# Optimization experiments

Hardware: AMD Instinct MI355X
Metric: run time of the kernel (lower is better)

## Reference

```python
import jax, jax.numpy as jnp
import numpy as np

B, A, D, H = 2048, 32, 128, 256

def setup_inputs() -> dict:
    key = jax.random.key(0)
    ks = jax.random.split(key, 12)
    s = lambda fan_in: 1.0 / np.sqrt(fan_in)
    return {
        "obs": jax.random.normal(ks[0], (B, A, D), dtype=jnp.float32),
        "act": jax.random.normal(ks[1], (B, A, 8), dtype=jnp.float32),
        "enc_W": jax.random.uniform(ks[2], (H, D), jnp.float32, -s(D), s(D)),
        "enc_b": jax.random.uniform(ks[3], (H,), jnp.float32, -s(D), s(D)),
        "fobs_W": jax.random.uniform(ks[4], (H, H), jnp.float32, -s(H), s(H)),
        "fobs_b": jax.random.uniform(ks[5], (H,), jnp.float32, -s(H), s(H)),
        "W_ih": jax.random.uniform(ks[6], (3 * H, H), jnp.float32, -s(H), s(H)),
        "b_ih": jax.random.uniform(ks[7], (3 * H,), jnp.float32, -s(H), s(H)),
        "W_hh": jax.random.uniform(ks[8], (3 * H, H), jnp.float32, -s(H), s(H)),
        "b_hh": jax.random.uniform(ks[9], (3 * H,), jnp.float32, -s(H), s(H)),
        "dec_W": jax.random.uniform(ks[10], (1, H), jnp.float32, -s(H), s(H)),
        "dec_b": jax.random.uniform(ks[11], (1,), jnp.float32, -s(H), s(H)),
    }

def _gru_cell(x, h, W_ih, b_ih, W_hh, b_hh):
    # torch.nn.GRUCell: gates stacked as [reset, update, new]
    gi = x @ W_ih.T + b_ih          # [N, 3H]
    gh = h @ W_hh.T + b_hh          # [N, 3H]
    i_r, i_z, i_n = jnp.split(gi, 3, axis=-1)
    h_r, h_z, h_n = jnp.split(gh, 3, axis=-1)
    r = jax.nn.sigmoid(i_r + h_r)
    z = jax.nn.sigmoid(i_z + h_z)
    n = jnp.tanh(i_n + r * h_n)
    return (1.0 - z) * n + z * h

def reference(obs, act, enc_W, enc_b, fobs_W, fobs_b, W_ih, b_ih, W_hh, b_hh, dec_W, dec_b):
    b, a, d = obs.shape
    x = obs.reshape(b * a, d)                         # [B*A, D]
    e = jax.nn.relu(x @ enc_W.T + enc_b)              # encoder + ReLU
    h = e @ fobs_W.T + fobs_b                         # h_out
    # k = 0: comm input is zeros
    h = _gru_cell(jnp.zeros_like(h), h, W_ih, b_ih, W_hh, b_hh)
    # k = 1: masked mean over other agents == (sum_j h_j - h_i) / n_agents
    hA = h.reshape(b, a, -1)                          # [B, A, H]
    c = (hA.sum(axis=1, keepdims=True) - hA) / a      # [B, A, H]
    h = _gru_cell(c.reshape(b * a, -1), h, W_ih, b_ih, W_hh, b_hh)
    return (h @ dec_W.T + dec_b).reshape(b, a, -1)    # [B, A, 1]
```

## Files before the change

### kernel.cpp

```cpp
#include <hip/hip_runtime.h>
#include <hip/hip_fp16.h>


#define NB   2048
#define NA   32
#define DIN  128
#define HID  256
#define SA   264

typedef _Float16 half8  __attribute__((ext_vector_type(8)));
typedef float    float4v __attribute__((ext_vector_type(4)));

#define ENC_OFF    0
#define FOBS_OFF   32768
#define WIH_OFF    98304
#define WHH_OFF    294912
#define PREP_TOTAL 491520

__global__ void prep_weights(const float* __restrict__ encW, const float* __restrict__ fobsW,
                             const float* __restrict__ wih,  const float* __restrict__ whh,
                             _Float16* __restrict__ prep) {
    int F = blockIdx.x * 256 + threadIdx.x;
    if (F >= PREP_TOTAL) return;
    const float* src; int K, NT, local = F;
    if (F < FOBS_OFF)     { src = encW;  K = 128; NT = 16; }
    else if (F < WIH_OFF) { src = fobsW; K = 256; NT = 16; local = F - FOBS_OFF; }
    else if (F < WHH_OFF) { src = wih;   K = 256; NT = 48; local = F - WIH_OFF; }
    else                  { src = whh;   K = 256; NT = 48; local = F - WHH_OFF; }
    int j    = local & 7;
    int lane = (local >> 3) & 63;
    int t    = local >> 9;
    int nt   = t % NT;
    int ks   = t / NT;
    int col  = nt * 16 + (lane & 15);
    int k    = ks * 32 + ((lane >> 4) << 3) + j;
    prep[F] = (_Float16)src[col * K + k];
}

__device__ __forceinline__ float sigmoid_f(float x) {
    x = fminf(fmaxf(x, -30.f), 30.f);
    return 1.f / (1.f + __expf(-x));
}
__device__ __forceinline__ float tanh_f(float x) {
    x = fminf(fmaxf(x, -15.f), 15.f);
    float e = __expf(-2.f * x);
    return (1.f - e) / (1.f + e);
}

__device__ __forceinline__ void zero22(float4v a[2][2]) {
    float4v z = {0.f, 0.f, 0.f, 0.f};
    a[0][0] = z; a[0][1] = z; a[1][0] = z; a[1][1] = z;
}

__device__ __forceinline__ half8 ldB(const _Float16* __restrict__ prepm, int NT, int nt, int ks,
                                     const float* __restrict__ raw, int K, int use_prep, int lane) {
    if (use_prep)
        return *(const half8*)(prepm + (((ks * NT + nt) * 64 + lane) << 3));
    half8 b;
    int l16 = lane & 15, kq = (lane >> 4) << 3;
    #pragma unroll
    for (int j = 0; j < 8; j++)
        b[j] = (_Float16)raw[(nt * 16 + l16) * K + ks * 32 + kq + j];
    return b;
}

template<int KSTEPS>
__device__ __forceinline__ void gemm_tile(const _Float16* __restrict__ Abuf,
        const _Float16* __restrict__ prepm, int NT, int ntg0,
        const float* __restrict__ raw, int K, int use_prep,
        int lane, float4v acc[2][2])
{
    const int l16 = lane & 15;
    const int kq  = (lane >> 4) << 3;
    #pragma unroll
    for (int ks = 0; ks < KSTEPS; ks++) {
        int kbase = ks * 32 + kq;
        half8 a0 = *(const half8*)(Abuf + l16 * SA + kbase);
        half8 a1 = *(const half8*)(Abuf + (16 + l16) * SA + kbase);
        half8 b0 = ldB(prepm, NT, ntg0,     ks, raw, K, use_prep, lane);
        half8 b1 = ldB(prepm, NT, ntg0 + 1, ks, raw, K, use_prep, lane);
        acc[0][0] = __builtin_amdgcn_mfma_f32_16x16x32_f16(a0, b0, acc[0][0], 0, 0, 0);
        acc[0][1] = __builtin_amdgcn_mfma_f32_16x16x32_f16(a0, b1, acc[0][1], 0, 0, 0);
        acc[1][0] = __builtin_amdgcn_mfma_f32_16x16x32_f16(a1, b0, acc[1][0], 0, 0, 0);
        acc[1][1] = __builtin_amdgcn_mfma_f32_16x16x32_f16(a1, b1, acc[1][1], 0, 0, 0);
    }
}

__global__ __launch_bounds__(512) void commnet_fused(
    const float* __restrict__ obs, const _Float16* __restrict__ prep,
    const float* __restrict__ enc_b, const float* __restrict__ fobs_b,
    const float* __restrict__ b_ih, const float* __restrict__ b_hh,
    const float* __restrict__ dec_W, const float* __restrict__ dec_b,
    float* __restrict__ out,
    const float* __restrict__ encW, const float* __restrict__ fobsW,
    const float* __restrict__ wih, const float* __restrict__ whh,
    int use_prep)
{
    const int b    = blockIdx.x;
    const int tid  = threadIdx.x;
    const int lane = tid & 63;
    const int w    = tid >> 6;
    const int l16  = lane & 15;
    const int quad = lane >> 4;
    const int kq   = quad << 3;
    const int ntl0 = w * 2;

    __shared__ __align__(16) _Float16 sA[2][NA * SA];
    __shared__ __align__(16) float S[HID];

    {
        const float* obsb = obs + (size_t)b * NA * DIN;
        int r   = tid >> 4;
        int off = (tid & 15) << 3;
        const float* src = obsb + r * DIN + off;
        float4v v0 = *(const float4v*)(src);
        float4v v1 = *(const float4v*)(src + 4);
        half8 hv;
        hv[0] = (_Float16)v0[0]; hv[1] = (_Float16)v0[1];
        hv[2] = (_Float16)v0[2]; hv[3] = (_Float16)v0[3];
        hv[4] = (_Float16)v1[0]; hv[5] = (_Float16)v1[1];
        hv[6] = (_Float16)v1[2]; hv[7] = (_Float16)v1[3];
        *(half8*)(&sA[0][r * SA + off]) = hv;
    }
    __syncthreads();

    float4v acc[2][2];

    zero22(acc);
    gemm_tile<4>(&sA[0][0], prep + ENC_OFF, 16, ntl0, encW, DIN, use_prep, lane, acc);
    #pragma unroll
    for (int nn = 0; nn < 2; nn++) {
        int col = (ntl0 + nn) * 16 + l16;
        float bb = enc_b[col];
        #pragma unroll
        for (int mt = 0; mt < 2; mt++)
            #pragma unroll
            for (int r = 0; r < 4; r++) {
                int row = mt * 16 + quad * 4 + r;
                float v = acc[mt][nn][r] + bb;
                sA[1][row * SA + col] = (_Float16)fmaxf(v, 0.f);
            }
    }
    __syncthreads();

    zero22(acc);
    gemm_tile<8>(&sA[1][0], prep + FOBS_OFF, 16, ntl0, fobsW, HID, use_prep, lane, acc);
    #pragma unroll
    for (int nn = 0; nn < 2; nn++) {
        int col = (ntl0 + nn) * 16 + l16;
        float bb = fobs_b[col];
        #pragma unroll
        for (int mt = 0; mt < 2; mt++)
            #pragma unroll
            for (int r = 0; r < 4; r++) {
                int row = mt * 16 + quad * 4 + r;
                sA[0][row * SA + col] = (_Float16)(acc[mt][nn][r] + bb);
            }
    }
    __syncthreads();

    {
        float4v aR[2][2], aZ[2][2], aN[2][2];
        zero22(aR); zero22(aZ); zero22(aN);
        #pragma unroll 2
        for (int ks = 0; ks < 8; ks++) {
            const int kbase = ks * 32 + kq;
            half8 a0 = *(const half8*)(&sA[0][l16 * SA + kbase]);
            half8 a1 = *(const half8*)(&sA[0][(16 + l16) * SA + kbase]);
            half8 bR0 = ldB(prep + WHH_OFF, 48,  0 + ntl0,     ks, whh, HID, use_prep, lane);
            half8 bR1 = ldB(prep + WHH_OFF, 48,  0 + ntl0 + 1, ks, whh, HID, use_prep, lane);
            half8 bZ0 = ldB(prep + WHH_OFF, 48, 16 + ntl0,     ks, whh, HID, use_prep, lane);
            half8 bZ1 = ldB(prep + WHH_OFF, 48, 16 + ntl0 + 1, ks, whh, HID, use_prep, lane);
            half8 bN0 = ldB(prep + WHH_OFF, 48, 32 + ntl0,     ks, whh, HID, use_prep, lane);
            half8 bN1 = ldB(prep + WHH_OFF, 48, 32 + ntl0 + 1, ks, whh, HID, use_prep, lane);
            aR[0][0] = __builtin_amdgcn_mfma_f32_16x16x32_f16(a0, bR0, aR[0][0], 0, 0, 0);
            aR[0][1] = __builtin_amdgcn_mfma_f32_16x16x32_f16(a0, bR1, aR[0][1], 0, 0, 0);
            aR[1][0] = __builtin_amdgcn_mfma_f32_16x16x32_f16(a1, bR0, aR[1][0], 0, 0, 0);
            aR[1][1] = __builtin_amdgcn_mfma_f32_16x16x32_f16(a1, bR1, aR[1][1], 0, 0, 0);
            aZ[0][0] = __builtin_amdgcn_mfma_f32_16x16x32_f16(a0, bZ0, aZ[0][0], 0, 0, 0);
            aZ[0][1] = __builtin_amdgcn_mfma_f32_16x16x32_f16(a0, bZ1, aZ[0][1], 0, 0, 0);
            aZ[1][0] = __builtin_amdgcn_mfma_f32_16x16x32_f16(a1, bZ0, aZ[1][0], 0, 0, 0);
            aZ[1][1] = __builtin_amdgcn_mfma_f32_16x16x32_f16(a1, bZ1, aZ[1][1], 0, 0, 0);
            aN[0][0] = __builtin_amdgcn_mfma_f32_16x16x32_f16(a0, bN0, aN[0][0], 0, 0, 0);
            aN[0][1] = __builtin_amdgcn_mfma_f32_16x16x32_f16(a0, bN1, aN[0][1], 0, 0, 0);
            aN[1][0] = __builtin_amdgcn_mfma_f32_16x16x32_f16(a1, bN0, aN[1][0], 0, 0, 0);
            aN[1][1] = __builtin_amdgcn_mfma_f32_16x16x32_f16(a1, bN1, aN[1][1], 0, 0, 0);
        }
        #pragma unroll
        for (int nn = 0; nn < 2; nn++) {
            int col = (ntl0 + nn) * 16 + l16;
            float biR = b_ih[col],       bhR = b_hh[col];
            float biZ = b_ih[256 + col], bhZ = b_hh[256 + col];
            float biN = b_ih[512 + col], bhN = b_hh[512 + col];
            float ssum = 0.f;
            #pragma unroll
            for (int mt = 0; mt < 2; mt++)
                #pragma unroll
                for (int r = 0; r < 4; r++) {
                    int row = mt * 16 + quad * 4 + r;
                    float rg = sigmoid_f(biR + aR[mt][nn][r] + bhR);
                    float zg = sigmoid_f(biZ + aZ[mt][nn][r] + bhZ);
                    float ng = tanh_f(biN + rg * (aN[mt][nn][r] + bhN));
                    float hold = (float)sA[0][row * SA + col];
                    float h1 = (1.f - zg) * ng + zg * hold;
                    sA[1][row * SA + col] = (_Float16)h1;
                    ssum += h1;
                }
            ssum += __shfl_xor(ssum, 16);
            ssum += __shfl_xor(ssum, 32);
            if (lane < 16) S[col] = ssum;
        }
    }
    __syncthreads();

    for (int i = tid; i < (NA * HID) / 8; i += 512) {
        int r  = i >> 5;
        int c8 = (i & 31) << 3;
        half8 hv = *(const half8*)(&sA[1][r * SA + c8]);
        float4v s0 = *(const float4v*)(&S[c8]);
        float4v s1 = *(const float4v*)(&S[c8 + 4]);
        half8 cv;
        cv[0] = (_Float16)((s0[0] - (float)hv[0]) * (1.f / 32.f));
        cv[1] = (_Float16)((s0[1] - (float)hv[1]) * (1.f / 32.f));
        cv[2] = (_Float16)((s0[2] - (float)hv[2]) * (1.f / 32.f));
        cv[3] = (_Float16)((s0[3] - (float)hv[3]) * (1.f / 32.f));
        cv[4] = (_Float16)((s1[0] - (float)hv[4]) * (1.f / 32.f));
        cv[5] = (_Float16)((s1[1] - (float)hv[5]) * (1.f / 32.f));
        cv[6] = (_Float16)((s1[2] - (float)hv[6]) * (1.f / 32.f));
        cv[7] = (_Float16)((s1[3] - (float)hv[7]) * (1.f / 32.f));
        *(half8*)(&sA[0][r * SA + c8]) = cv;
    }
    __syncthreads();
    if (tid < NA) S[tid] = 0.f;
    __syncthreads();

    {
        float4v aR[2][2], aZ[2][2], aNi[2][2], aNh[2][2];
        zero22(aR); zero22(aZ); zero22(aNi); zero22(aNh);
        #pragma unroll 2
        for (int ks = 0; ks < 8; ks++) {
            const int kbase = ks * 32 + kq;
            half8 c0 = *(const half8*)(&sA[0][l16 * SA + kbase]);
            half8 c1 = *(const half8*)(&sA[0][(16 + l16) * SA + kbase]);
            half8 bIR0 = ldB(prep + WIH_OFF, 48,  0 + ntl0,     ks, wih, HID, use_prep, lane);
            half8 bIR1 = ldB(prep + WIH_OFF, 48,  0 + ntl0 + 1, ks, wih, HID, use_prep, lane);
            half8 bIZ0 = ldB(prep + WIH_OFF, 48, 16 + ntl0,     ks, wih, HID, use_prep, lane);
            half8 bIZ1 = ldB(prep + WIH_OFF, 48, 16 + ntl0 + 1, ks, wih, HID, use_prep, lane);
            half8 bIN0 = ldB(prep + WIH_OFF, 48, 32 + ntl0,     ks, wih, HID, use_prep, lane);
            half8 bIN1 = ldB(prep + WIH_OFF, 48, 32 + ntl0 + 1, ks, wih, HID, use_prep, lane);
            aR[0][0]  = __builtin_amdgcn_mfma_f32_16x16x32_f16(c0, bIR0, aR[0][0], 0, 0, 0);
            aR[0][1]  = __builtin_amdgcn_mfma_f32_16x16x32_f16(c0, bIR1, aR[0][1], 0, 0, 0);
            aR[1][0]  = __builtin_amdgcn_mfma_f32_16x16x32_f16(c1, bIR0, aR[1][0], 0, 0, 0);
            aR[1][1]  = __builtin_amdgcn_mfma_f32_16x16x32_f16(c1, bIR1, aR[1][1], 0, 0, 0);
            aZ[0][0]  = __builtin_amdgcn_mfma_f32_16x16x32_f16(c0, bIZ0, aZ[0][0], 0, 0, 0);
            aZ[0][1]  = __builtin_amdgcn_mfma_f32_16x16x32_f16(c0, bIZ1, aZ[0][1], 0, 0, 0);
            aZ[1][0]  = __builtin_amdgcn_mfma_f32_16x16x32_f16(c1, bIZ0, aZ[1][0], 0, 0, 0);
            aZ[1][1]  = __builtin_amdgcn_mfma_f32_16x16x32_f16(c1, bIZ1, aZ[1][1], 0, 0, 0);
            aNi[0][0] = __builtin_amdgcn_mfma_f32_16x16x32_f16(c0, bIN0, aNi[0][0], 0, 0, 0);
            aNi[0][1] = __builtin_amdgcn_mfma_f32_16x16x32_f16(c0, bIN1, aNi[0][1], 0, 0, 0);
            aNi[1][0] = __builtin_amdgcn_mfma_f32_16x16x32_f16(c1, bIN0, aNi[1][0], 0, 0, 0);
            aNi[1][1] = __builtin_amdgcn_mfma_f32_16x16x32_f16(c1, bIN1, aNi[1][1], 0, 0, 0);
            half8 h0 = *(const half8*)(&sA[1][l16 * SA + kbase]);
            half8 h1f = *(const half8*)(&sA[1][(16 + l16) * SA + kbase]);
            half8 bHR0 = ldB(prep + WHH_OFF, 48,  0 + ntl0,     ks, whh, HID, use_prep, lane);
            half8 bHR1 = ldB(prep + WHH_OFF, 48,  0 + ntl0 + 1, ks, whh, HID, use_prep, lane);
            half8 bHZ0 = ldB(prep + WHH_OFF, 48, 16 + ntl0,     ks, whh, HID, use_prep, lane);
            half8 bHZ1 = ldB(prep + WHH_OFF, 48, 16 + ntl0 + 1, ks, whh, HID, use_prep, lane);
            half8 bHN0 = ldB(prep + WHH_OFF, 48, 32 + ntl0,     ks, whh, HID, use_prep, lane);
            half8 bHN1 = ldB(prep + WHH_OFF, 48, 32 + ntl0 + 1, ks, whh, HID, use_prep, lane);
            aR[0][0]  = __builtin_amdgcn_mfma_f32_16x16x32_f16(h0,  bHR0, aR[0][0], 0, 0, 0);
            aR[0][1]  = __builtin_amdgcn_mfma_f32_16x16x32_f16(h0,  bHR1, aR[0][1], 0, 0, 0);
            aR[1][0]  = __builtin_amdgcn_mfma_f32_16x16x32_f16(h1f, bHR0, aR[1][0], 0, 0, 0);
            aR[1][1]  = __builtin_amdgcn_mfma_f32_16x16x32_f16(h1f, bHR1, aR[1][1], 0, 0, 0);
            aZ[0][0]  = __builtin_amdgcn_mfma_f32_16x16x32_f16(h0,  bHZ0, aZ[0][0], 0, 0, 0);
            aZ[0][1]  = __builtin_amdgcn_mfma_f32_16x16x32_f16(h0,  bHZ1, aZ[0][1], 0, 0, 0);
            aZ[1][0]  = __builtin_amdgcn_mfma_f32_16x16x32_f16(h1f, bHZ0, aZ[1][0], 0, 0, 0);
            aZ[1][1]  = __builtin_amdgcn_mfma_f32_16x16x32_f16(h1f, bHZ1, aZ[1][1], 0, 0, 0);
            aNh[0][0] = __builtin_amdgcn_mfma_f32_16x16x32_f16(h0,  bHN0, aNh[0][0], 0, 0, 0);
            aNh[0][1] = __builtin_amdgcn_mfma_f32_16x16x32_f16(h0,  bHN1, aNh[0][1], 0, 0, 0);
            aNh[1][0] = __builtin_amdgcn_mfma_f32_16x16x32_f16(h1f, bHN0, aNh[1][0], 0, 0, 0);
            aNh[1][1] = __builtin_amdgcn_mfma_f32_16x16x32_f16(h1f, bHN1, aNh[1][1], 0, 0, 0);
        }

        float dw0 = dec_W[(ntl0    ) * 16 + l16];
        float dw1 = dec_W[(ntl0 + 1) * 16 + l16];
        float p[2][4];
        #pragma unroll
        for (int mt = 0; mt < 2; mt++)
            #pragma unroll
            for (int r = 0; r < 4; r++)
                p[mt][r] = 0.f;
        #pragma unroll
        for (int nn = 0; nn < 2; nn++) {
            int col = (ntl0 + nn) * 16 + l16;
            float biR = b_ih[col],       bhR = b_hh[col];
            float biZ = b_ih[256 + col], bhZ = b_hh[256 + col];
            float biN = b_ih[512 + col], bhN = b_hh[512 + col];
            float dw = nn ? dw1 : dw0;
            #pragma unroll
            for (int mt = 0; mt < 2; mt++)
                #pragma unroll
                for (int r = 0; r < 4; r++) {
                    int row = mt * 16 + quad * 4 + r;
                    float rg = sigmoid_f(aR[mt][nn][r] + biR + bhR);
                    float zg = sigmoid_f(aZ[mt][nn][r] + biZ + bhZ);
                    float ng = tanh_f((aNi[mt][nn][r] + biN) + rg * (aNh[mt][nn][r] + bhN));
                    float h1v = (float)sA[1][row * SA + col];
                    float h2 = (1.f - zg) * ng + zg * h1v;
                    p[mt][r] += h2 * dw;
                }
        }
        #pragma unroll
        for (int m = 1; m <= 8; m <<= 1) {
            #pragma unroll
            for (int mt = 0; mt < 2; mt++)
                #pragma unroll
                for (int r = 0; r < 4; r++)
                    p[mt][r] += __shfl_xor(p[mt][r], m);
        }
        if (l16 == 0) {
            #pragma unroll
            for (int mt = 0; mt < 2; mt++)
                #pragma unroll
                for (int r = 0; r < 4; r++)
                    atomicAdd(&S[mt * 16 + quad * 4 + r], p[mt][r]);
        }
    }
    __syncthreads();
    if (tid < NA) out[(size_t)b * NA + tid] = S[tid] + dec_b[0];
}

extern "C" void kernel_launch(void* const* d_in, const int* in_sizes, int n_in,
                              void* d_out, int out_size, void* d_ws, size_t ws_size,
                              hipStream_t stream) {
    const float* obs   = (const float*)d_in[0];
    const float* encW  = (const float*)d_in[2];
    const float* encb  = (const float*)d_in[3];
    const float* fobsW = (const float*)d_in[4];
    const float* fobsb = (const float*)d_in[5];
    const float* wih   = (const float*)d_in[6];
    const float* bih   = (const float*)d_in[7];
    const float* whh   = (const float*)d_in[8];
    const float* bhh   = (const float*)d_in[9];
    const float* decW  = (const float*)d_in[10];
    const float* decb  = (const float*)d_in[11];
    float* out = (float*)d_out;

    _Float16* prep = (_Float16*)d_ws;
    int use_prep = (ws_size >= (size_t)PREP_TOTAL * sizeof(_Float16)) ? 1 : 0;
    if (use_prep) {
        prep_weights<<<(PREP_TOTAL + 255) / 256, 256, 0, stream>>>(encW, fobsW, wih, whh, prep);
    }
    commnet_fused<<<NB, 512, 0, stream>>>(obs, prep, encb, fobsb, bih, bhh, decW, decb, out,
                                          encW, fobsW, wih, whh, use_prep);
}
```

Before: 275.5 us.

## Process two batch elements per 1024-thread block to halve grid size

```diff
diff --git a/kernel.cpp b/kernel.cpp
--- a/kernel.cpp
+++ b/kernel.cpp
@@ -7,6 +7,7 @@
 #define DIN  128
 #define HID  256
 #define SA   264
+#define MROWS 64
 
 typedef _Float16 half8  __attribute__((ext_vector_type(8)));
 typedef float    float4v __attribute__((ext_vector_type(4)));
@@ -72,7 +73,7 @@
 {
     const int l16 = lane & 15;
     const int kq  = (lane >> 4) << 3;
-    #pragma unroll
+    #pragma unroll 2
     for (int ks = 0; ks < KSTEPS; ks++) {
         int kbase = ks * 32 + kq;
         half8 a0 = *(const half8*)(Abuf + l16 * SA + kbase);
@@ -86,7 +87,7 @@
     }
 }
 
-__global__ __launch_bounds__(512) void commnet_fused(
+__global__ __launch_bounds__(1024) void commnet_fused(
     const float* __restrict__ obs, const _Float16* __restrict__ prep,
     const float* __restrict__ enc_b, const float* __restrict__ fobs_b,
     const float* __restrict__ b_ih, const float* __restrict__ b_hh,
@@ -100,16 +101,20 @@
     const int tid  = threadIdx.x;
     const int lane = tid & 63;
     const int w    = tid >> 6;
+    const int wr   = w >> 3;
+    const int wc   = w & 7;
     const int l16  = lane & 15;
     const int quad = lane >> 4;
     const int kq   = quad << 3;
-    const int ntl0 = w * 2;
-
-    __shared__ __align__(16) _Float16 sA[2][NA * SA];
-    __shared__ __align__(16) float S[HID];
-
-    {
-        const float* obsb = obs + (size_t)b * NA * DIN;
+    const int ntg0 = wc * 2;
+    const int rowB = wr * 32;
+
+    __shared__ __align__(16) _Float16 sA[2][MROWS * SA];
+    __shared__ __align__(16) float S[2][HID];
+    __shared__ float Srow[MROWS];
+
+    {
+        const float* obsb = obs + (size_t)b * MROWS * DIN;
         int r   = tid >> 4;
         int off = (tid & 15) << 3;
         const float* src = obsb + r * DIN + off;
@@ -126,36 +131,39 @@
 
     float4v acc[2][2];
 
-    zero22(acc);
-    gemm_tile<4>(&sA[0][0], prep + ENC_OFF, 16, ntl0, encW, DIN, use_prep, lane, acc);
-    #pragma unroll
-    for (int nn = 0; nn < 2; nn++) {
-        int col = (ntl0 + nn) * 16 + l16;
-        float bb = enc_b[col];
-        #pragma unroll
-        for (int mt = 0; mt < 2; mt++)
-            #pragma unroll
-            for (int r = 0; r < 4; r++) {
-                int row = mt * 16 + quad * 4 + r;
-                float v = acc[mt][nn][r] + bb;
-                sA[1][row * SA + col] = (_Float16)fmaxf(v, 0.f);
-            }
-    }
-    __syncthreads();
-
-    zero22(acc);
-    gemm_tile<8>(&sA[1][0], prep + FOBS_OFF, 16, ntl0, fobsW, HID, use_prep, lane, acc);
-    #pragma unroll
-    for (int nn = 0; nn < 2; nn++) {
-        int col = (ntl0 + nn) * 16 + l16;
-        float bb = fobs_b[col];
-        #pragma unroll
-        for (int mt = 0; mt < 2; mt++)
-            #pragma unroll
-            for (int r = 0; r < 4; r++) {
-                int row = mt * 16 + quad * 4 + r;
-                sA[0][row * SA + col] = (_Float16)(acc[mt][nn][r] + bb);
-            }
+    {
+        zero22(acc);
+        gemm_tile<4>(&sA[0][rowB * SA], prep + ENC_OFF, 16, ntg0, encW, DIN, use_prep, lane, acc);
+        #pragma unroll
+        for (int nt = 0; nt < 2; nt++) {
+            int col = wc * 32 + nt * 16 + l16;
+            float bb = enc_b[col];
+            #pragma unroll
+            for (int mt = 0; mt < 2; mt++)
+                #pragma unroll
+                for (int r = 0; r < 4; r++) {
+                    int row = rowB + mt * 16 + quad * 4 + r;
+                    sA[1][row * SA + col] = (_Float16)fmaxf(acc[mt][nt][r] + bb, 0.f);
+                }
+        }
+    }
+    __syncthreads();
+
+    {
+        zero22(acc);
+        gemm_tile<8>(&sA[1][rowB * SA], prep + FOBS_OFF, 16, ntg0, fobsW, HID, use_prep, lane, acc);
+        #pragma unroll
+        for (int nt = 0; nt < 2; nt++) {
+            int col = wc * 32 + nt * 16 + l16;
+            float bb = fobs_b[col];
+            #pragma unroll
+            for (int mt = 0; mt < 2; mt++)
+                #pragma unroll
+                for (int r = 0; r < 4; r++) {
+                    int row = rowB + mt * 16 + quad * 4 + r;
+                    sA[0][row * SA + col] = (_Float16)(acc[mt][nt][r] + bb);
+                }
+        }
     }
     __syncthreads();
 
@@ -165,125 +173,131 @@
         #pragma unroll 2
         for (int ks = 0; ks < 8; ks++) {
             const int kbase = ks * 32 + kq;
-            half8 a0 = *(const half8*)(&sA[0][l16 * SA + kbase]);
-            half8 a1 = *(const half8*)(&sA[0][(16 + l16) * SA + kbase]);
-            half8 bR0 = ldB(prep + WHH_OFF, 48,  0 + ntl0,     ks, whh, HID, use_prep, lane);
-            half8 bR1 = ldB(prep + WHH_OFF, 48,  0 + ntl0 + 1, ks, whh, HID, use_prep, lane);
-            half8 bZ0 = ldB(prep + WHH_OFF, 48, 16 + ntl0,     ks, whh, HID, use_prep, lane);
-            half8 bZ1 = ldB(prep + WHH_OFF, 48, 16 + ntl0 + 1, ks, whh, HID, use_prep, lane);
-            half8 bN0 = ldB(prep + WHH_OFF, 48, 32 + ntl0,     ks, whh, HID, use_prep, lane);
-            half8 bN1 = ldB(prep + WHH_OFF, 48, 32 + ntl0 + 1, ks, whh, HID, use_prep, lane);
+            half8 a0 = *(const half8*)(&sA[0][(rowB + l16) * SA + kbase]);
+            half8 a1 = *(const half8*)(&sA[0][(rowB + 16 + l16) * SA + kbase]);
+            half8 bR0 = ldB(prep + WHH_OFF, 48,  0 + ntg0,     ks, whh, HID, use_prep, lane);
+            half8 bR1 = ldB(prep + WHH_OFF, 48,  0 + ntg0 + 1, ks, whh, HID, use_prep, lane);
             aR[0][0] = __builtin_amdgcn_mfma_f32_16x16x32_f16(a0, bR0, aR[0][0], 0, 0, 0);
             aR[0][1] = __builtin_amdgcn_mfma_f32_16x16x32_f16(a0, bR1, aR[0][1], 0, 0, 0);
             aR[1][0] = __builtin_amdgcn_mfma_f32_16x16x32_f16(a1, bR0, aR[1][0], 0, 0, 0);
             aR[1][1] = __builtin_amdgcn_mfma_f32_16x16x32_f16(a1, bR1, aR[1][1], 0, 0, 0);
+            half8 bZ0 = ldB(prep + WHH_OFF, 48, 16 + ntg0,     ks, whh, HID, use_prep, lane);
+            half8 bZ1 = ldB(prep + WHH_OFF, 48, 16 + ntg0 + 1, ks, whh, HID, use_prep, lane);
             aZ[0][0] = __builtin_amdgcn_mfma_f32_16x16x32_f16(a0, bZ0, aZ[0][0], 0, 0, 0);
             aZ[0][1] = __builtin_amdgcn_mfma_f32_16x16x32_f16(a0, bZ1, aZ[0][1], 0, 0, 0);
             aZ[1][0] = __builtin_amdgcn_mfma_f32_16x16x32_f16(a1, bZ0, aZ[1][0], 0, 0, 0);
             aZ[1][1] = __builtin_amdgcn_mfma_f32_16x16x32_f16(a1, bZ1, aZ[1][1], 0, 0, 0);
+            half8 bN0 = ldB(prep + WHH_OFF, 48, 32 + ntg0,     ks, whh, HID, use_prep, lane);
+            half8 bN1 = ldB(prep + WHH_OFF, 48, 32 + ntg0 + 1, ks, whh, HID, use_prep, lane);
             aN[0][0] = __builtin_amdgcn_mfma_f32_16x16x32_f16(a0, bN0, aN[0][0], 0, 0, 0);
             aN[0][1] = __builtin_amdgcn_mfma_f32_16x16x32_f16(a0, bN1, aN[0][1], 0, 0, 0);
             aN[1][0] = __builtin_amdgcn_mfma_f32_16x16x32_f16(a1, bN0, aN[1][0], 0, 0, 0);
             aN[1][1] = __builtin_amdgcn_mfma_f32_16x16x32_f16(a1, bN1, aN[1][1], 0, 0, 0);
         }
         #pragma unroll
-        for (int nn = 0; nn < 2; nn++) {
-            int col = (ntl0 + nn) * 16 + l16;
+        for (int nt = 0; nt < 2; nt++) {
+            int col = wc * 32 + nt * 16 + l16;
             float biR = b_ih[col],       bhR = b_hh[col];
             float biZ = b_ih[256 + col], bhZ = b_hh[256 + col];
             float biN = b_ih[512 + col], bhN = b_hh[512 + col];
-            float ssum = 0.f;
+            float psum = 0.f;
             #pragma unroll
             for (int mt = 0; mt < 2; mt++)
                 #pragma unroll
                 for (int r = 0; r < 4; r++) {
-                    int row = mt * 16 + quad * 4 + r;
-                    float rg = sigmoid_f(biR + aR[mt][nn][r] + bhR);
-                    float zg = sigmoid_f(biZ + aZ[mt][nn][r] + bhZ);
-                    float ng = tanh_f(biN + rg * (aN[mt][nn][r] + bhN));
+                    int row = rowB + mt * 16 + quad * 4 + r;
+                    float rg = sigmoid_f(biR + aR[mt][nt][r] + bhR);
+                    float zg = sigmoid_f(biZ + aZ[mt][nt][r] + bhZ);
+                    float ng = tanh_f(biN + rg * (aN[mt][nt][r] + bhN));
                     float hold = (float)sA[0][row * SA + col];
                     float h1 = (1.f - zg) * ng + zg * hold;
                     sA[1][row * SA + col] = (_Float16)h1;
-                    ssum += h1;
+                    psum += h1;
                 }
-            ssum += __shfl_xor(ssum, 16);
-            ssum += __shfl_xor(ssum, 32);
-            if (lane < 16) S[col] = ssum;
-        }
-    }
-    __syncthreads();
-
-    for (int i = tid; i < (NA * HID) / 8; i += 512) {
-        int r  = i >> 5;
-        int c8 = (i & 31) << 3;
-        half8 hv = *(const half8*)(&sA[1][r * SA + c8]);
-        float4v s0 = *(const float4v*)(&S[c8]);
-        float4v s1 = *(const float4v*)(&S[c8 + 4]);
-        half8 cv;
-        cv[0] = (_Float16)((s0[0] - (float)hv[0]) * (1.f / 32.f));
-        cv[1] = (_Float16)((s0[1] - (float)hv[1]) * (1.f / 32.f));
-        cv[2] = (_Float16)((s0[2] - (float)hv[2]) * (1.f / 32.f));
-        cv[3] = (_Float16)((s0[3] - (float)hv[3]) * (1.f / 32.f));
-        cv[4] = (_Float16)((s1[0] - (float)hv[4]) * (1.f / 32.f));
-        cv[5] = (_Float16)((s1[1] - (float)hv[5]) * (1.f / 32.f));
-        cv[6] = (_Float16)((s1[2] - (float)hv[6]) * (1.f / 32.f));
-        cv[7] = (_Float16)((s1[3] - (float)hv[7]) * (1.f / 32.f));
-        *(half8*)(&sA[0][r * SA + c8]) = cv;
-    }
-    __syncthreads();
-    if (tid < NA) S[tid] = 0.f;
+            psum += __shfl_xor(psum, 16);
+            psum += __shfl_xor(psum, 32);
+            if (lane < 16) S[wr][wc * 32 + nt * 16 + lane] = psum;
+        }
+    }
+    __syncthreads();
+
+    {
+        #pragma unroll
+        for (int it = 0; it < 2; it++) {
+            int i  = tid + it * 1024;
+            int r  = i >> 5;
+            int c8 = (i & 31) << 3;
+            const float* Sp = &S[r >> 5][0];
+            half8 hv = *(const half8*)(&sA[1][r * SA + c8]);
+            float4v t0 = *(const float4v*)(Sp + c8);
+            float4v t1 = *(const float4v*)(Sp + c8 + 4);
+            half8 cv;
+            cv[0] = (_Float16)((t0[0] - (float)hv[0]) * (1.f / 32.f));
+            cv[1] = (_Float16)((t0[1] - (float)hv[1]) * (1.f / 32.f));
+            cv[2] = (_Float16)((t0[2] - (float)hv[2]) * (1.f / 32.f));
+            cv[3] = (_Float16)((t0[3] - (float)hv[3]) * (1.f / 32.f));
+            cv[4] = (_Float16)((t1[0] - (float)hv[4]) * (1.f / 32.f));
+            cv[5] = (_Float16)((t1[1] - (float)hv[5]) * (1.f / 32.f));
+            cv[6] = (_Float16)((t1[2] - (float)hv[6]) * (1.f / 32.f));
+            cv[7] = (_Float16)((t1[3] - (float)hv[7]) * (1.f / 32.f));
+            *(half8*)(&sA[0][r * SA + c8]) = cv;
+        }
+        if (tid < MROWS) Srow[tid] = 0.f;
+    }
     __syncthreads();
 
     {
         float4v aR[2][2], aZ[2][2], aNi[2][2], aNh[2][2];
         zero22(aR); zero22(aZ); zero22(aNi); zero22(aNh);
-        #pragma unroll 2
+        #pragma unroll 1
         for (int ks = 0; ks < 8; ks++) {
             const int kbase = ks * 32 + kq;
-            half8 c0 = *(const half8*)(&sA[0][l16 * SA + kbase]);
-            half8 c1 = *(const half8*)(&sA[0][(16 + l16) * SA + kbase]);
-            half8 bIR0 = ldB(prep + WIH_OFF, 48,  0 + ntl0,     ks, wih, HID, use_prep, lane);
-            half8 bIR1 = ldB(prep + WIH_OFF, 48,  0 + ntl0 + 1, ks, wih, HID, use_prep, lane);
-            half8 bIZ0 = ldB(prep + WIH_OFF, 48, 16 + ntl0,     ks, wih, HID, use_prep, lane);
-            half8 bIZ1 = ldB(prep + WIH_OFF, 48, 16 + ntl0 + 1, ks, wih, HID, use_prep, lane);
-            half8 bIN0 = ldB(prep + WIH_OFF, 48, 32 + ntl0,     ks, wih, HID, use_prep, lane);
-            half8 bIN1 = ldB(prep + WIH_OFF, 48, 32 + ntl0 + 1, ks, wih, HID, use_prep, lane);
-            aR[0][0]  = __builtin_amdgcn_mfma_f32_16x16x32_f16(c0, bIR0, aR[0][0], 0, 0, 0);
-            aR[0][1]  = __builtin_amdgcn_mfma_f32_16x16x32_f16(c0, bIR1, aR[0][1], 0, 0, 0);
-            aR[1][0]  = __builtin_amdgcn_mfma_f32_16x16x32_f16(c1, bIR0, aR[1][0], 0, 0, 0);
-            aR[1][1]  = __builtin_amdgcn_mfma_f32_16x16x32_f16(c1, bIR1, aR[1][1], 0, 0, 0);
-            aZ[0][0]  = __builtin_amdgcn_mfma_f32_16x16x32_f16(c0, bIZ0, aZ[0][0], 0, 0, 0);
-            aZ[0][1]  = __builtin_amdgcn_mfma_f32_16x16x32_f16(c0, bIZ1, aZ[0][1], 0, 0, 0);
-            aZ[1][0]  = __builtin_amdgcn_mfma_f32_16x16x32_f16(c1, bIZ0, aZ[1][0], 0, 0, 0);
-            aZ[1][1]  = __builtin_amdgcn_mfma_f32_16x16x32_f16(c1, bIZ1, aZ[1][1], 0, 0, 0);
-            aNi[0][0] = __builtin_amdgcn_mfma_f32_16x16x32_f16(c0, bIN0, aNi[0][0], 0, 0, 0);
-            aNi[0][1] = __builtin_amdgcn_mfma_f32_16x16x32_f16(c0, bIN1, aNi[0][1], 0, 0, 0);
-            aNi[1][0] = __builtin_amdgcn_mfma_f32_16x16x32_f16(c1, bIN0, aNi[1][0], 0, 0, 0);
-            aNi[1][1] = __builtin_amdgcn_mfma_f32_16x16x32_f16(c1, bIN1, aNi[1][1], 0, 0, 0);
-            half8 h0 = *(const half8*)(&sA[1][l16 * SA + kbase]);
-            half8 h1f = *(const half8*)(&sA[1][(16 + l16) * SA + kbase]);
-            half8 bHR0 = ldB(prep + WHH_OFF, 48,  0 + ntl0,     ks, whh, HID, use_prep, lane);
-            half8 bHR1 = ldB(prep + WHH_OFF, 48,  0 + ntl0 + 1, ks, whh, HID, use_prep, lane);
-            half8 bHZ0 = ldB(prep + WHH_OFF, 48, 16 + ntl0,     ks, whh, HID, use_prep, lane);
-            half8 bHZ1 = ldB(prep + WHH_OFF, 48, 16 + ntl0 + 1, ks, whh, HID, use_prep, lane);
-            half8 bHN0 = ldB(prep + WHH_OFF, 48, 32 + ntl0,     ks, whh, HID, use_prep, lane);
-            half8 bHN1 = ldB(prep + WHH_OFF, 48, 32 + ntl0 + 1, ks, whh, HID, use_prep, lane);
-            aR[0][0]  = __builtin_amdgcn_mfma_f32_16x16x32_f16(h0,  bHR0, aR[0][0], 0, 0, 0);
-            aR[0][1]  = __builtin_amdgcn_mfma_f32_16x16x32_f16(h0,  bHR1, aR[0][1], 0, 0, 0);
-            aR[1][0]  = __builtin_amdgcn_mfma_f32_16x16x32_f16(h1f, bHR0, aR[1][0], 0, 0, 0);
-            aR[1][1]  = __builtin_amdgcn_mfma_f32_16x16x32_f16(h1f, bHR1, aR[1][1], 0, 0, 0);
-            aZ[0][0]  = __builtin_amdgcn_mfma_f32_16x16x32_f16(h0,  bHZ0, aZ[0][0], 0, 0, 0);
-            aZ[0][1]  = __builtin_amdgcn_mfma_f32_16x16x32_f16(h0,  bHZ1, aZ[0][1], 0, 0, 0);
-            aZ[1][0]  = __builtin_amdgcn_mfma_f32_16x16x32_f16(h1f, bHZ0, aZ[1][0], 0, 0, 0);
-            aZ[1][1]  = __builtin_amdgcn_mfma_f32_16x16x32_f16(h1f, bHZ1, aZ[1][1], 0, 0, 0);
-            aNh[0][0] = __builtin_amdgcn_mfma_f32_16x16x32_f16(h0,  bHN0, aNh[0][0], 0, 0, 0);
-            aNh[0][1] = __builtin_amdgcn_mfma_f32_16x16x32_f16(h0,  bHN1, aNh[0][1], 0, 0, 0);
-            aNh[1][0] = __builtin_amdgcn_mfma_f32_16x16x32_f16(h1f, bHN0, aNh[1][0], 0, 0, 0);
-            aNh[1][1] = __builtin_amdgcn_mfma_f32_16x16x32_f16(h1f, bHN1, aNh[1][1], 0, 0, 0);
-        }
-
-        float dw0 = dec_W[(ntl0    ) * 16 + l16];
-        float dw1 = dec_W[(ntl0 + 1) * 16 + l16];
+            {
+                half8 c0 = *(const half8*)(&sA[0][(rowB + l16) * SA + kbase]);
+                half8 c1 = *(const half8*)(&sA[0][(rowB + 16 + l16) * SA + kbase]);
+                half8 bR0 = ldB(prep + WIH_OFF, 48,  0 + ntg0,     ks, wih, HID, use_prep, lane);
+                half8 bR1 = ldB(prep + WIH_OFF, 48,  0 + ntg0 + 1, ks, wih, HID, use_prep, lane);
+                aR[0][0]  = __builtin_amdgcn_mfma_f32_16x16x32_f16(c0, bR0, aR[0][0], 0, 0, 0);
+                aR[0][1]  = __builtin_amdgcn_mfma_f32_16x16x32_f16(c0, bR1, aR[0][1], 0, 0, 0);
+                aR[1][0]  = __builtin_amdgcn_mfma_f32_16x16x32_f16(c1, bR0, aR[1][0], 0, 0, 0);
+                aR[1][1]  = __builtin_amdgcn_mfma_f32_16x16x32_f16(c1, bR1, aR[1][1], 0, 0, 0);
+                half8 bZ0 = ldB(prep + WIH_OFF, 48, 16 + ntg0,     ks, wih, HID, use_prep, lane);
+                half8 bZ1 = ldB(prep + WIH_OFF, 48, 16 + ntg0 + 1, ks, wih, HID, use_prep, lane);
+                aZ[0][0]  = __builtin_amdgcn_mfma_f32_16x16x32_f16(c0, bZ0, aZ[0][0], 0, 0, 0);
+                aZ[0][1]  = __builtin_amdgcn_mfma_f32_16x16x32_f16(c0, bZ1, aZ[0][1], 0, 0, 0);
+                aZ[1][0]  = __builtin_amdgcn_mfma_f32_16x16x32_f16(c1, bZ0, aZ[1][0], 0, 0, 0);
+                aZ[1][1]  = __builtin_amdgcn_mfma_f32_16x16x32_f16(c1, bZ1, aZ[1][1], 0, 0, 0);
+                half8 bN0 = ldB(prep + WIH_OFF, 48, 32 + ntg0,     ks, wih, HID, use_prep, lane);
+                half8 bN1 = ldB(prep + WIH_OFF, 48, 32 + ntg0 + 1, ks, wih, HID, use_prep, lane);
+                aNi[0][0] = __builtin_amdgcn_mfma_f32_16x16x32_f16(c0, bN0, aNi[0][0], 0, 0, 0);
+                aNi[0][1] = __builtin_amdgcn_mfma_f32_16x16x32_f16(c0, bN1, aNi[0][1], 0, 0, 0);
+                aNi[1][0] = __builtin_amdgcn_mfma_f32_16x16x32_f16(c1, bN0, aNi[1][0], 0, 0, 0);
+                aNi[1][1] = __builtin_amdgcn_mfma_f32_16x16x32_f16(c1, bN1, aNi[1][1], 0, 0, 0);
+            }
+            {
+                half8 h0 = *(const half8*)(&sA[1][(rowB + l16) * SA + kbase]);
+                half8 h1f = *(const half8*)(&sA[1][(rowB + 16 + l16) * SA + kbase]);
+                half8 bR0 = ldB(prep + WHH_OFF, 48,  0 + ntg0,     ks, whh, HID, use_prep, lane);
+                half8 bR1 = ldB(prep + WHH_OFF, 48,  0 + ntg0 + 1, ks, whh, HID, use_prep, lane);
+                aR[0][0]  = __builtin_amdgcn_mfma_f32_16x16x32_f16(h0,  bR0, aR[0][0], 0, 0, 0);
+                aR[0][1]  = __builtin_amdgcn_mfma_f32_16x16x32_f16(h0,  bR1, aR[0][1], 0, 0, 0);
+                aR[1][0]  = __builtin_amdgcn_mfma_f32_16x16x32_f16(h1f, bR0, aR[1][0], 0, 0, 0);
+                aR[1][1]  = __builtin_amdgcn_mfma_f32_16x16x32_f16(h1f, bR1, aR[1][1], 0, 0, 0);
+                half8 bZ0 = ldB(prep + WHH_OFF, 48, 16 + ntg0,     ks, whh, HID, use_prep, lane);
+                half8 bZ1 = ldB(prep + WHH_OFF, 48, 16 + ntg0 + 1, ks, whh, HID, use_prep, lane);
+                aZ[0][0]  = __builtin_amdgcn_mfma_f32_16x16x32_f16(h0,  bZ0, aZ[0][0], 0, 0, 0);
+                aZ[0][1]  = __builtin_amdgcn_mfma_f32_16x16x32_f16(h0,  bZ1, aZ[0][1], 0, 0, 0);
+                aZ[1][0]  = __builtin_amdgcn_mfma_f32_16x16x32_f16(h1f, bZ0, aZ[1][0], 0, 0, 0);
+                aZ[1][1]  = __builtin_amdgcn_mfma_f32_16x16x32_f16(h1f, bZ1, aZ[1][1], 0, 0, 0);
+                half8 bN0 = ldB(prep + WHH_OFF, 48, 32 + ntg0,     ks, whh, HID, use_prep, lane);
+                half8 bN1 = ldB(prep + WHH_OFF, 48, 32 + ntg0 + 1, ks, whh, HID, use_prep, lane);
+                aNh[0][0] = __builtin_amdgcn_mfma_f32_16x16x32_f16(h0,  bN0, aNh[0][0], 0, 0, 0);
+                aNh[0][1] = __builtin_amdgcn_mfma_f32_16x16x32_f16(h0,  bN1, aNh[0][1], 0, 0, 0);
+                aNh[1][0] = __builtin_amdgcn_mfma_f32_16x16x32_f16(h1f, bN0, aNh[1][0], 0, 0, 0);
+                aNh[1][1] = __builtin_amdgcn_mfma_f32_16x16x32_f16(h1f, bN1, aNh[1][1], 0, 0, 0);
+            }
+        }
+
         float p[2][4];
         #pragma unroll
         for (int mt = 0; mt < 2; mt++)
@@ -291,20 +305,20 @@
             for (int r = 0; r < 4; r++)
                 p[mt][r] = 0.f;
         #pragma unroll
-        for (int nn = 0; nn < 2; nn++) {
-            int col = (ntl0 + nn) * 16 + l16;
+        for (int nt = 0; nt < 2; nt++) {
+            int col = wc * 32 + nt * 16 + l16;
             float biR = b_ih[col],       bhR = b_hh[col];
             float biZ = b_ih[256 + col], bhZ = b_hh[256 + col];
             float biN = b_ih[512 + col], bhN = b_hh[512 + col];
-            float dw = nn ? dw1 : dw0;
+            float dw  = dec_W[col];
             #pragma unroll
             for (int mt = 0; mt < 2; mt++)
                 #pragma unroll
                 for (int r = 0; r < 4; r++) {
-                    int row = mt * 16 + quad * 4 + r;
-                    float rg = sigmoid_f(aR[mt][nn][r] + biR + bhR);
-                    float zg = sigmoid_f(aZ[mt][nn][r] + biZ + bhZ);
-                    float ng = tanh_f((aNi[mt][nn][r] + biN) + rg * (aNh[mt][nn][r] + bhN));
+                    int row = rowB + mt * 16 + quad * 4 + r;
+                    float rg = sigmoid_f(aR[mt][nt][r] + biR + bhR);
+                    float zg = sigmoid_f(aZ[mt][nt][r] + biZ + bhZ);
+                    float ng = tanh_f((aNi[mt][nt][r] + biN) + rg * (aNh[mt][nt][r] + bhN));
                     float h1v = (float)sA[1][row * SA + col];
                     float h2 = (1.f - zg) * ng + zg * h1v;
                     p[mt][r] += h2 * dw;
@@ -323,11 +337,11 @@
             for (int mt = 0; mt < 2; mt++)
                 #pragma unroll
                 for (int r = 0; r < 4; r++)
-                    atomicAdd(&S[mt * 16 + quad * 4 + r], p[mt][r]);
-        }
-    }
-    __syncthreads();
-    if (tid < NA) out[(size_t)b * NA + tid] = S[tid] + dec_b[0];
+                    atomicAdd(&Srow[rowB + mt * 16 + quad * 4 + r], p[mt][r]);
+        }
+    }
+    __syncthreads();
+    if (tid < MROWS) out[(size_t)b * MROWS + tid] = Srow[tid] + dec_b[0];
 }
 
 extern "C" void kernel_launch(void* const* d_in, const int* in_sizes, int n_in,
@@ -351,6 +365,6 @@
     if (use_prep) {
         prep_weights<<<(PREP_TOTAL + 255) / 256, 256, 0, stream>>>(encW, fobsW, wih, whh, prep);
     }
-    commnet_fused<<<NB, 512, 0, stream>>>(obs, prep, encb, fobsb, bih, bhh, decW, decb, out,
-                                          encW, fobsW, wih, whh, use_prep);
-}
+    commnet_fused<<<NB / 2, 1024, 0, stream>>>(obs, prep, encb, fobsb, bih, bhh, decW, decb, out,
+                                               encW, fobsW, wih, whh, use_prep);
+}
```

Measured after the change: 324.2 us. +17.7%, slower.
